# Optimization experiments

Measured on AMD Instinct MI355X. Metric: run time of the kernel, lower is better.

Reference implementation:

```python
import jax, jax.numpy as jnp
import numpy as np

B, S, WD, H, STEP = 32, 512, 512, 512, 2
NG = 8  # gate order: f1, f2, f3, f4, f5, i, o, u


def setup_inputs() -> dict:
    key = jax.random.key(0)
    ks = jax.random.split(key, 12)
    std = 0.1
    word_inputs = jax.random.normal(ks[0], (B, S, WD), jnp.float32)
    position_table = jax.random.randint(ks[1], (B, S), 0, S + 1)  # 0 -> pad row
    mask = jnp.ones((B, S), jnp.int32)
    # nograd uniform(-0.05, 0.05) initial states created inside torch forward
    init_h = jax.random.uniform(ks[2], (B, S, H), jnp.float32, -0.05, 0.05)
    init_c = jax.random.uniform(ks[3], (B, S, H), jnp.float32, -0.05, 0.05)
    Wx = std * jax.random.normal(ks[4], (NG, H, H), jnp.float32)
    Wh = std * jax.random.normal(ks[5], (NG, 2 * H, H), jnp.float32)
    Wi = std * jax.random.normal(ks[6], (NG, WD, H), jnp.float32)
    Wd = std * jax.random.normal(ks[7], (NG, H, H), jnp.float32)
    Ws = std * jax.random.normal(ks[8], (NG, H, H), jnp.float32)
    b = std * jax.random.normal(ks[9], (NG, H), jnp.float32)
    gW = std * jax.random.normal(ks[10], (6, H, H), jnp.float32)  # Wxd,Whd,Wxo,Who,Wxf,Whf
    gb = std * jax.random.normal(ks[11], (3, H), jnp.float32)     # bd,bo,bf
    return dict(word_inputs=word_inputs, init_h=init_h, init_c=init_c,
                Wx=Wx, Wh=Wh, Wi=Wi, Wd=Wd, Ws=Ws, b=b, gW=gW, gb=gb,
                position_table=position_table, mask=mask, num_layers=4)


def _shift_sum_before(x, steps):
    # sum_{s=1..steps} of x right-shifted by s with zero padding at front
    out = jnp.zeros_like(x)
    for s in range(1, steps + 1):
        pad = jnp.zeros(x[:, :s].shape, x.dtype)
        out = out + jnp.concatenate([pad, x[:, :-s]], axis=1)
    return out


def _shift_sum_after(x, steps):
    out = jnp.zeros_like(x)
    for s in range(1, steps + 1):
        pad = jnp.zeros(x[:, :s].shape, x.dtype)
        out = out + jnp.concatenate([x[:, s:], pad], axis=1)
    return out


def _position_switch(x, pos):
    # prepend a zero pad row at position 0, then gather along seq dim
    x_add = jnp.concatenate([jnp.zeros_like(x[:, :1]), x], axis=1)  # [B,S+1,H]
    return jnp.take_along_axis(x_add, pos[:, :, None], axis=1)


def reference(word_inputs, init_h, init_c, Wx, Wh, Wi, Wd, Ws, b, gW, gb,
              position_table, mask, num_layers):
    maskf = mask.astype(jnp.float32)
    seq_mask = maskf[:, :, None]                         # [B,S,1]
    mask_score = (maskf * 1e25 - 1e25)[:, :, None]       # 0 where valid, -1e25 where pad
    emb = (word_inputs * seq_mask).reshape(-1, WD)       # embedding_hidden_state_pre
    h = init_h * seq_mask
    c = init_c * seq_mask
    dummy_h = jnp.mean(h, axis=1)
    dummy_c = jnp.mean(c, axis=1)
    gWxd, gWhd, gWxo, gWho, gWxf, gWhf = gW[0], gW[1], gW[2], gW[3], gW[4], gW[5]
    gbd, gbo, gbf = gb[0], gb[1], gb[2]
    for _ in range(num_layers):
        sw_h = _position_switch(h, position_table)
        sw_c = _position_switch(c, position_table)
        combined = jnp.mean(h, axis=1)                   # [B,H]
        rh = h.reshape(-1, H)                            # [B*S,H]
        td_h = jnp.broadcast_to(dummy_h[:, None], h.shape).reshape(-1, H)
        # dummy (sentence-state) node update
        gd = jax.nn.sigmoid(dummy_h @ gWxd + combined @ gWhd + gbd)
        go = jax.nn.sigmoid(dummy_h @ gWxo + combined @ gWho + gbo)
        gf = jax.nn.sigmoid(td_h @ gWxf + rh @ gWhf + gbf).reshape(h.shape) + mask_score
        scores = jax.nn.softmax(jnp.concatenate([gf, gd[:, None]], axis=1), axis=1)  # [B,S+1,H]
        dummy_c_new = jnp.sum(scores[:, :S] * c, axis=1) + scores[:, S] * dummy_c
        dummy_h_new = go * jnp.tanh(dummy_c_new)
        # neighbor window sums (before/after) for h and c
        hb = _shift_sum_before(h, STEP).reshape(-1, H)
        ha = _shift_sum_after(h, STEP).reshape(-1, H)
        cb = _shift_sum_before(c, STEP).reshape(-1, H)
        ca = _shift_sum_after(c, STEP).reshape(-1, H)
        cat = jnp.concatenate([hb, ha], axis=1)          # [B*S,2H]
        td_c = jnp.broadcast_to(dummy_c[:, None], c.shape).reshape(-1, H)
        sw_hf = sw_h.reshape(-1, H)
        sw_cf = sw_c.reshape(-1, H)
        # all 8 gate pre-activations in stacked einsums: [8,B*S,H]
        z = (jnp.einsum('nh,ghk->gnk', rh, Wx)
             + jnp.einsum('nd,gdk->gnk', cat, Wh)
             + jnp.einsum('nw,gwk->gnk', emb, Wi)
             + jnp.einsum('nh,ghk->gnk', td_h, Wd)
             + jnp.einsum('nh,ghk->gnk', sw_hf, Ws)
             + b[:, None, :])
        gates6 = jax.nn.softmax(jax.nn.sigmoid(z[:6]), axis=0)  # normalize f1..f5,i
        f1, f2, f3, f4, f5, i_t = gates6[0], gates6[1], gates6[2], gates6[3], gates6[4], gates6[5]
        o_t = jax.nn.sigmoid(z[6])
        u_t = jnp.tanh(z[7])
        cf = c.reshape(-1, H)
        c_new = f1 * cb + f2 * ca + f3 * cf + f4 * td_c + f5 * sw_cf + i_t * u_t
        h_new = o_t * jnp.tanh(c_new)
        h = h_new.reshape(B, S, H) * seq_mask
        c = c_new.reshape(B, S, H) * seq_mask
        dummy_h, dummy_c = dummy_h_new, dummy_c_new
    return h
```

## Files before the change

kernel.cpp:

```cpp
#include <hip/hip_runtime.h>
#include <cstddef>

#define Bn 32
#define Sn 512
#define Hn 512
#define Rn (Bn*Sn)
#define NLAYER 4
constexpr size_t NHe = (size_t)Rn * Hn;

typedef __attribute__((ext_vector_type(8))) _Float16 f16x8;
typedef __attribute__((ext_vector_type(4))) float f32x4;

__device__ __forceinline__ float sigf(float x) { return 1.f / (1.f + __expf(-x)); }
__device__ __forceinline__ void gl_lds16(const void* g, void* l) {
  __builtin_amdgcn_global_load_lds((const __attribute__((address_space(1))) void*)g,
                                   (__attribute__((address_space(3))) void*)l, 16, 0, 0);
}
#define VMCNT(n) asm volatile("s_waitcnt vmcnt(" #n ")" ::: "memory")

__global__ void k_init(const float* __restrict__ ih, const float* __restrict__ ic,
                       const int* __restrict__ mask,
                       float* __restrict__ h, float* __restrict__ c) {
  size_t i = (size_t)blockIdx.x * blockDim.x + threadIdx.x;
  size_t n = i >> 7;
  float m = (float)mask[n];
  float4 b = ((const float4*)ih)[i];
  float4 d = ((const float4*)ic)[i];
  b.x *= m; b.y *= m; b.z *= m; b.w *= m;
  d.x *= m; d.y *= m; d.z *= m; d.w *= m;
  ((float4*)h)[i] = b; ((float4*)c)[i] = d;
}

__global__ void k_mean2(const float* __restrict__ x, const float* __restrict__ y,
                        float* __restrict__ ox, float* __restrict__ oy) {
  int idx = blockIdx.x * blockDim.x + threadIdx.x;
  int b = idx >> 9, k = idx & 511;
  const float* px = x + (size_t)b * Sn * Hn + k;
  const float* py = y + (size_t)b * Sn * Hn + k;
  float sx = 0.f, sy = 0.f;
#pragma unroll 8
  for (int t = 0; t < Sn; ++t) { sx += px[(size_t)t * Hn]; sy += py[(size_t)t * Hn]; }
  ox[idx] = sx * (1.f / Sn); oy[idx] = sy * (1.f / Sn);
}

__global__ void k_mean1a(const float* __restrict__ x, float* __restrict__ part) {
  int b = blockIdx.x, sc = blockIdx.y;
  int k4 = threadIdx.x & 127;
  int so = threadIdx.x >> 7;
  const float4* px = (const float4*)x + ((size_t)(b * Sn + sc * 64 + so)) * 128 + k4;
  float4 s = make_float4(0.f, 0.f, 0.f, 0.f);
#pragma unroll 4
  for (int t = 0; t < 32; ++t) {
    float4 v = px[(size_t)t * 256];
    s.x += v.x; s.y += v.y; s.z += v.z; s.w += v.w;
  }
  ((float4*)part)[((size_t)(sc * 2 + so) * Bn + b) * 128 + k4] = s;
}
__global__ void k_mean1b(const float* __restrict__ part, float* __restrict__ comb) {
  int idx = blockIdx.x * blockDim.x + threadIdx.x;
  int b = idx >> 7, k4 = idx & 127;
  float4 s = make_float4(0.f, 0.f, 0.f, 0.f);
#pragma unroll
  for (int p = 0; p < 16; ++p) {
    float4 v = ((const float4*)part)[((size_t)p * Bn + b) * 128 + k4];
    s.x += v.x; s.y += v.y; s.z += v.z; s.w += v.w;
  }
  s.x *= (1.f / Sn); s.y *= (1.f / Sn); s.z *= (1.f / Sn); s.w *= (1.f / Sn);
  ((float4*)comb)[idx] = s;
}

__global__ void k_gates_small(const float* __restrict__ dh, const float* __restrict__ comb,
                              const float* __restrict__ gW, const float* __restrict__ gb,
                              float* __restrict__ gd, float* __restrict__ go,
                              float* __restrict__ gfA) {
  int idx = blockIdx.x * blockDim.x + threadIdx.x;
  int b = idx >> 9, k = idx & 511;
  const float* gW0 = gW;
  const float* gW1 = gW + 1 * Hn * Hn;
  const float* gW2 = gW + 2 * Hn * Hn;
  const float* gW3 = gW + 3 * Hn * Hn;
  const float* gW4 = gW + 4 * Hn * Hn;
  const float* dhb = dh + b * Hn;
  const float* cbp = comb + b * Hn;
  float s0 = 0.f, s1 = 0.f, s2 = 0.f, s3 = 0.f, s4 = 0.f;
#pragma unroll 4
  for (int j = 0; j < Hn; ++j) {
    float a = dhb[j], c2 = cbp[j];
    s0 += a * gW0[j * Hn + k];
    s1 += c2 * gW1[j * Hn + k];
    s2 += a * gW2[j * Hn + k];
    s3 += c2 * gW3[j * Hn + k];
    s4 += a * gW4[j * Hn + k];
  }
  gd[idx] = sigf(s0 + s1 + gb[k]);
  go[idx] = sigf(s2 + s3 + gb[Hn + k]);
  gfA[idx] = s4 + gb[2 * Hn + k];
}

__global__ void k_dWd(const float* __restrict__ dh, const float* __restrict__ Wd,
                      float* __restrict__ dWd) {
  int idx = blockIdx.x * blockDim.x + threadIdx.x;
  int k = idx & 511; int bg = idx >> 9; int b = bg & 31; int g = bg >> 5;
  const float* w = Wd + (size_t)g * Hn * Hn;
  const float* dhb = dh + b * Hn;
  float s = 0.f;
#pragma unroll 4
  for (int j = 0; j < Hn; ++j) s += dhb[j] * w[j * Hn + k];
  dWd[idx] = s;
}

__global__ void k_dummy1(const float* __restrict__ G, const float* __restrict__ gfA,
                         const float* __restrict__ c, const int* __restrict__ mask,
                         float* __restrict__ np_, float* __restrict__ dp_) {
  int b = blockIdx.x, sc = blockIdx.y;
  int k = threadIdx.x;
  float gfa = gfA[(b << 9) | k];
  const float* Gp = G + ((size_t)(b * Sn + sc * 64)) * Hn + k;
  const float* cp = c + ((size_t)(b * Sn + sc * 64)) * Hn + k;
  const int* mp = mask + b * Sn + sc * 64;
  float num = 0.f, den = 0.f;
#pragma unroll 4
  for (int s = 0; s < 64; ++s) {
    float e = __expf(sigf(Gp[(size_t)s * Hn] + gfa));
    e = mp[s] ? e : 0.f;
    num += e * cp[(size_t)s * Hn];
    den += e;
  }
  np_[((size_t)sc * Bn + b) * Hn + k] = num;
  dp_[((size_t)sc * Bn + b) * Hn + k] = den;
}
__global__ void k_dummy2(const float* __restrict__ np_, const float* __restrict__ dp_,
                         const float* __restrict__ gd, const float* __restrict__ go,
                         const float* __restrict__ dc,
                         float* __restrict__ dh2, float* __restrict__ dc2) {
  int idx = blockIdx.x * blockDim.x + threadIdx.x;
  int b = idx >> 9, k = idx & 511;
  float ed = __expf(gd[idx]);
  float num = ed * dc[idx], den = ed;
#pragma unroll
  for (int sc = 0; sc < 8; ++sc) {
    num += np_[((size_t)sc * Bn + b) * Hn + k];
    den += dp_[((size_t)sc * Bn + b) * Hn + k];
  }
  float d = num / den;
  dc2[idx] = d;
  dh2[idx] = go[idx] * tanhf(d);
}

__global__ void k_convw(const float* __restrict__ Wx, const float* __restrict__ Wh,
                        const float* __restrict__ Wsm, const float* __restrict__ Wi,
                        _Float16* __restrict__ Bhat) {
  int kcT = blockIdx.x, nT = blockIdx.y, tg = blockIdx.z;
  int t = tg >> 3, g = tg & 7;
  const float* base;
  if (t == 0)      base = Wx  + (size_t)g * 262144;
  else if (t == 1) base = Wh  + (size_t)g * 524288;
  else if (t == 2) base = Wh  + (size_t)g * 524288 + 262144;
  else if (t == 3) base = Wsm + (size_t)g * 262144;
  else             base = Wi  + (size_t)g * 262144;
  size_t sbase = ((size_t)(t * 16 + nT) * 16 + kcT) * 8192 + (size_t)g * 1024;
  int lane = threadIdx.x;
  for (int cch = lane; cch < 128; cch += 64) {
    int ni = cch >> 6, quad = (cch >> 4) & 3, l15 = cch & 15;
    int n = nT * 32 + ni * 16 + l15;
    int k0 = kcT * 32 + quad * 8;
    f16x8 w8;
#pragma unroll
    for (int j = 0; j < 8; ++j) w8[j] = (_Float16)base[(size_t)(k0 + j) * Hn + n];
    *(f16x8*)&Bhat[sbase + (size_t)cch * 8] = w8;
  }
}

__global__ void k_convG(const float* __restrict__ gW, _Float16* __restrict__ Ghat) {
  int kcT = blockIdx.x, nT4 = blockIdx.y;
  int tid = threadIdx.x;
  const float* w = gW + (size_t)5 * Hn * Hn;
  size_t sb = ((size_t)(nT4 * 16 + kcT)) * 4096;
#pragma unroll
  for (int half = 0; half < 2; ++half) {
    int st = half * 256 + tid;
    int nj = st >> 6, quad = (st >> 4) & 3, l15 = st & 15;
    int n = nT4 * 128 + nj * 16 + l15;
    int k0 = kcT * 32 + quad * 8;
    f16x8 w8;
#pragma unroll
    for (int j = 0; j < 8; ++j) w8[j] = (_Float16)w[(size_t)(k0 + j) * Hn + n];
    *(f16x8*)&Ghat[sb + (size_t)st * 8] = w8;
  }
}

__global__ void k_prepA(const float* __restrict__ h, const int* __restrict__ pos,
                        _Float16* __restrict__ Ahat) {
  const int mb = blockIdx.x, kcT = blockIdx.y, t = blockIdx.z;
  const int tid = threadIdx.x;
  size_t sb = ((size_t)(t * 128 + mb) * 16 + kcT) * 4096;
#pragma unroll
  for (int half = 0; half < 2; ++half) {
    int st = half * 256 + tid;
    int rg = st >> 6, quad = (st >> 4) & 3, l15 = st & 15;
    int r = mb * 128 + rg * 16 + l15;
    int srow = r & (Sn - 1);
    int k0 = kcT * 32 + quad * 8;
    const float* base = h + (size_t)r * Hn + k0;
    float v[8];
    if (t == 0) {
#pragma unroll
      for (int j = 0; j < 8; ++j) v[j] = base[j];
    } else if (t == 1) {
#pragma unroll
      for (int j = 0; j < 8; ++j) v[j] = 0.f;
      if (srow >= 1) { const float* p = base - Hn;
#pragma unroll
        for (int j = 0; j < 8; ++j) v[j] += p[j]; }
      if (srow >= 2) { const float* p = base - 2 * Hn;
#pragma unroll
        for (int j = 0; j < 8; ++j) v[j] += p[j]; }
    } else if (t == 2) {
#pragma unroll
      for (int j = 0; j < 8; ++j) v[j] = 0.f;
      if (srow <= Sn - 2) { const float* p = base + Hn;
#pragma unroll
        for (int j = 0; j < 8; ++j) v[j] += p[j]; }
      if (srow <= Sn - 3) { const float* p = base + 2 * Hn;
#pragma unroll
        for (int j = 0; j < 8; ++j) v[j] += p[j]; }
    } else {
      int pp = pos[r];
      if (pp) {
        const float* p = h + ((size_t)((r >> 9) * Sn + pp - 1)) * Hn + k0;
#pragma unroll
        for (int j = 0; j < 8; ++j) v[j] = p[j];
      } else {
#pragma unroll
        for (int j = 0; j < 8; ++j) v[j] = 0.f;
      }
    }
    f16x8 o8;
#pragma unroll
    for (int j = 0; j < 8; ++j) o8[j] = (_Float16)v[j];
    *(f16x8*)&Ahat[sb + (size_t)st * 8] = o8;
  }
}

__global__ void k_prepW(const float* __restrict__ w, const int* __restrict__ mask,
                        _Float16* __restrict__ Ahat) {
  const int mb = blockIdx.x, kcT = blockIdx.y;
  const int tid = threadIdx.x;
  size_t sb = ((size_t)(4 * 128 + mb) * 16 + kcT) * 4096;
#pragma unroll
  for (int half = 0; half < 2; ++half) {
    int st = half * 256 + tid;
    int rg = st >> 6, quad = (st >> 4) & 3, l15 = st & 15;
    int r = mb * 128 + rg * 16 + l15;
    int k0 = kcT * 32 + quad * 8;
    float mf = (float)mask[r];
    const float* base = w + (size_t)r * Hn + k0;
    f16x8 o8;
#pragma unroll
    for (int j = 0; j < 8; ++j) o8[j] = (_Float16)(base[j] * mf);
    *(f16x8*)&Ahat[sb + (size_t)st * 8] = o8;
  }
}

__global__ __launch_bounds__(256, 3) void k_gemm1(const _Float16* __restrict__ Ahat,
                                                  const _Float16* __restrict__ Ghat,
                                                  float* __restrict__ G) {
  __shared__ _Float16 As[2][4096];
  __shared__ _Float16 Bs[2][4096];
  const int tid = threadIdx.x;
  const int mb = blockIdx.x, nT4 = blockIdx.y;
  const int lane = tid & 63, wid = tid >> 6;
  const int quad = lane >> 4, l15 = lane & 15;
  const int afo0 = (((wid * 2 + 0) * 4 + quad) * 16 + l15) * 8;
  const int afo1 = (((wid * 2 + 1) * 4 + quad) * 16 + l15) * 8;

  f32x4 acc[2][8];
#pragma unroll
  for (int mi = 0; mi < 2; ++mi)
#pragma unroll
    for (int nj = 0; nj < 8; ++nj) acc[mi][nj] = (f32x4){0.f, 0.f, 0.f, 0.f};

  auto stage = [&](int buf, int kcT) {
    const int4* sa = (const int4*)Ahat + ((size_t)(mb * 16 + kcT) << 9);
    const int4* sbp = (const int4*)Ghat + ((size_t)(nT4 * 16 + kcT) << 9);
#pragma unroll
    for (int q = 0; q < 2; ++q) {
      gl_lds16(sa + q * 256 + tid, &As[buf][(q * 256 + tid) * 8]);
      gl_lds16(sbp + q * 256 + tid, &Bs[buf][(q * 256 + tid) * 8]);
    }
  };

  stage(0, 0);
  __syncthreads();
#pragma unroll 1
  for (int kcT = 0; kcT < 16; ++kcT) {
    const int cur = kcT & 1;
    if (kcT < 15) stage(cur ^ 1, kcT + 1);
    f16x8 a0 = *(const f16x8*)&As[cur][afo0];
    f16x8 a1 = *(const f16x8*)&As[cur][afo1];
#pragma unroll
    for (int nj = 0; nj < 8; ++nj) {
      f16x8 bh = *(const f16x8*)&Bs[cur][((nj * 4 + quad) * 16 + l15) * 8];
      acc[0][nj] = __builtin_amdgcn_mfma_f32_16x16x32_f16(a0, bh, acc[0][nj], 0, 0, 0);
      acc[1][nj] = __builtin_amdgcn_mfma_f32_16x16x32_f16(a1, bh, acc[1][nj], 0, 0, 0);
    }
    __syncthreads();
  }
#pragma unroll
  for (int mi = 0; mi < 2; ++mi)
#pragma unroll
    for (int r = 0; r < 4; ++r) {
      int row = mb * 128 + wid * 32 + mi * 16 + quad * 4 + r;
      float* gp = G + (size_t)row * Hn + nT4 * 128 + l15;
#pragma unroll
      for (int nj = 0; nj < 8; ++nj) gp[nj * 16] = acc[mi][nj][r];
    }
}

__global__ __launch_bounds__(512, 2) void k_mega(
    const float* __restrict__ c,
    const _Float16* __restrict__ Ahat, const _Float16* __restrict__ Bhat,
    const int* __restrict__ pos, const int* __restrict__ mask,
    const float* __restrict__ dc, const float* __restrict__ dWd,
    const float* __restrict__ bias,
    float* __restrict__ hout, float* __restrict__ cout) {
  __shared__ _Float16 As[2][16384];
  __shared__ _Float16 Bs[2][16384];

  const int tid = threadIdx.x;
  const int id = blockIdx.x;
  const int xcd = id & 7;
  const int loc = id >> 3;
  const int mt = xcd * 8 + (loc >> 4);
  const int nT = loc & 15;
  const int m0 = mt * 256;
  const int n0 = nT * 32;
  const int bb = m0 >> 9;

  const int lane = tid & 63, wid = tid >> 6;
  const int quad = lane >> 4, l15 = lane & 15;
  const int row_grp = wid >> 1;
  const int col_half = wid & 1;
  const int mb2 = row_grp >> 1;
  const int rg0 = (row_grp & 1) * 4;

  const int afoA0 = (mb2 * 4096) + ((rg0 * 4 + quad) * 16 + l15) * 8;
  const int afoA1 = (2 * 4096 + mb2 * 4096) + ((rg0 * 4 + quad) * 16 + l15) * 8;
  const int bfo = col_half * 512 + quad * 128 + l15 * 8;

  f32x4 acc[8][4];
#pragma unroll
  for (int g = 0; g < 8; ++g)
#pragma unroll
    for (int mi = 0; mi < 4; ++mi) acc[g][mi] = (f32x4){0.f, 0.f, 0.f, 0.f};

  auto stageA = [&](int buf, int kt2) {
    const int t = kt2 >> 3, kc2 = (kt2 & 7) * 2;
#pragma unroll
    for (int kk = 0; kk < 2; ++kk)
#pragma unroll
      for (int m2 = 0; m2 < 2; ++m2) {
        const int4* src = (const int4*)Ahat +
            ((size_t)((t * 128 + mt * 2 + m2) * 16 + kc2 + kk)) * 512;
        gl_lds16(src + tid, &As[buf][(kk * 2 + m2) * 4096 + tid * 8]);
      }
#pragma unroll
    for (int kk = 0; kk < 2; ++kk) {
      const int4* srcb = (const int4*)Bhat +
          ((size_t)((t * 16 + nT) * 16 + kc2 + kk)) * 1024;
      gl_lds16(srcb + tid, &Bs[buf][kk * 8192 + tid * 8]);
    }
  };
  auto stageB = [&](int buf, int kt2) {
    const int t = kt2 >> 3, kc2 = (kt2 & 7) * 2;
#pragma unroll
    for (int kk = 0; kk < 2; ++kk) {
      const int4* srcb = (const int4*)Bhat +
          ((size_t)((t * 16 + nT) * 16 + kc2 + kk)) * 1024 + 512;
      gl_lds16(srcb + tid, &Bs[buf][kk * 8192 + 4096 + tid * 8]);
    }
  };

  stageA(0, 0);
  stageB(0, 0);

#pragma unroll 1
  for (int kt = 0; kt < 40; ++kt) {
    const int cur = kt & 1;
    const int nbuf = cur ^ 1;
    VMCNT(2);
    __builtin_amdgcn_s_barrier();
    f16x8 a[4][2], b[4];
#pragma unroll
    for (int mi = 0; mi < 4; ++mi) {
      a[mi][0] = *(const f16x8*)&As[cur][afoA0 + mi * 512];
      a[mi][1] = *(const f16x8*)&As[cur][afoA1 + mi * 512];
    }
#pragma unroll
    for (int g = 0; g < 4; ++g) b[g] = *(const f16x8*)&Bs[cur][g * 1024 + bfo];
    if (kt < 39) stageA(nbuf, kt + 1);
    asm volatile("s_waitcnt lgkmcnt(0)" ::: "memory");
    __builtin_amdgcn_sched_barrier(0);
    __builtin_amdgcn_s_setprio(1);
#pragma unroll
    for (int g = 0; g < 4; ++g) {
#pragma unroll
      for (int mi = 0; mi < 4; ++mi)
        acc[g][mi] = __builtin_amdgcn_mfma_f32_16x16x32_f16(a[mi][0], b[g], acc[g][mi], 0, 0, 0);
    }
    f16x8 b1[4];
#pragma unroll
    for (int g = 0; g < 4; ++g) b1[g] = *(const f16x8*)&Bs[cur][8192 + g * 1024 + bfo];
    asm volatile("s_waitcnt lgkmcnt(0)" ::: "memory");
    __builtin_amdgcn_sched_barrier(0);
#pragma unroll
    for (int g = 0; g < 4; ++g) {
#pragma unroll
      for (int mi = 0; mi < 4; ++mi)
        acc[g][mi] = __builtin_amdgcn_mfma_f32_16x16x32_f16(a[mi][1], b1[g], acc[g][mi], 0, 0, 0);
    }
    __builtin_amdgcn_s_setprio(0);
    if (kt < 39) { VMCNT(6); }
    else         { VMCNT(0); }
    __builtin_amdgcn_s_barrier();
    f16x8 c0[4], c1[4];
#pragma unroll
    for (int g = 0; g < 4; ++g) {
      c0[g] = *(const f16x8*)&Bs[cur][4096 + g * 1024 + bfo];
      c1[g] = *(const f16x8*)&Bs[cur][8192 + 4096 + g * 1024 + bfo];
    }
    if (kt < 39) stageB(nbuf, kt + 1);
    asm volatile("s_waitcnt lgkmcnt(0)" ::: "memory");
    __builtin_amdgcn_sched_barrier(0);
    __builtin_amdgcn_s_setprio(1);
#pragma unroll
    for (int g = 0; g < 4; ++g) {
#pragma unroll
      for (int mi = 0; mi < 4; ++mi)
        acc[4 + g][mi] = __builtin_amdgcn_mfma_f32_16x16x32_f16(a[mi][0], c0[g], acc[4 + g][mi], 0, 0, 0);
    }
#pragma unroll
    for (int g = 0; g < 4; ++g) {
#pragma unroll
      for (int mi = 0; mi < 4; ++mi)
        acc[4 + g][mi] = __builtin_amdgcn_mfma_f32_16x16x32_f16(a[mi][1], c1[g], acc[4 + g][mi], 0, 0, 0);
    }
    __builtin_amdgcn_s_setprio(0);
    __builtin_amdgcn_s_barrier();
  }

  const int col = n0 + col_half * 16 + l15;
  const float tdcv = dc[bb * Hn + col];
  float biasr[8], dwdr[8];
#pragma unroll
  for (int g = 0; g < 8; ++g) {
    biasr[g] = bias[g * Hn + col];
    dwdr[g] = dWd[((size_t)g * Bn + bb) * Hn + col];
  }

#pragma unroll
  for (int mi = 0; mi < 4; ++mi) {
#pragma unroll
    for (int r = 0; r < 4; ++r) {
      const int row = m0 + row_grp * 64 + mi * 16 + quad * 4 + r;
      const int srow = row & (Sn - 1);
      const float mf = (float)mask[row];
      const int pp = pos[row];
      const size_t rb = (size_t)row * Hn;
      float cf = c[rb + col];
      float cb = 0.f, ca = 0.f;
      if (srow >= 1) cb = c[rb - Hn + col];
      if (srow >= 2) cb += c[rb - 2 * Hn + col];
      if (srow <= Sn - 2) ca = c[rb + Hn + col];
      if (srow <= Sn - 3) ca += c[rb + 2 * Hn + col];
      float sw = pp ? c[((size_t)(bb * Sn + pp - 1)) * Hn + col] : 0.f;
      float z[8];
#pragma unroll
      for (int g = 0; g < 8; ++g)
        z[g] = acc[g][mi][r] + biasr[g] + dwdr[g];
      float e0 = __expf(sigf(z[0]));
      float e1 = __expf(sigf(z[1]));
      float e2 = __expf(sigf(z[2]));
      float e3 = __expf(sigf(z[3]));
      float e4 = __expf(sigf(z[4]));
      float e5 = __expf(sigf(z[5]));
      float inv = 1.f / (e0 + e1 + e2 + e3 + e4 + e5);
      float o = sigf(z[6]);
      float u = tanhf(z[7]);
      float cn = inv * (e0 * cb + e1 * ca + e2 * cf + e3 * tdcv + e4 * sw + e5 * u);
      cout[rb + col] = cn * mf;
      hout[rb + col] = o * tanhf(cn) * mf;
    }
  }
}

extern "C" void kernel_launch(void* const* d_in, const int* in_sizes, int n_in,
                              void* d_out, int out_size, void* d_ws, size_t ws_size,
                              hipStream_t stream) {
  (void)in_sizes; (void)n_in; (void)out_size; (void)ws_size;
  const float* word   = (const float*)d_in[0];
  const float* init_h = (const float*)d_in[1];
  const float* init_c = (const float*)d_in[2];
  const float* Wx     = (const float*)d_in[3];
  const float* Wh     = (const float*)d_in[4];
  const float* Wi     = (const float*)d_in[5];
  const float* Wdm    = (const float*)d_in[6];
  const float* Wsm    = (const float*)d_in[7];
  const float* bias   = (const float*)d_in[8];
  const float* gW     = (const float*)d_in[9];
  const float* gb     = (const float*)d_in[10];
  const int*   pos    = (const int*)d_in[11];
  const int*   mask   = (const int*)d_in[12];

  float* ws = (float*)d_ws;
  size_t off = 0;
  auto alloc = [&](size_t nel) { float* p = ws + off; off += nel; return p; };
  float* cA   = alloc(NHe);
  float* cB   = alloc(NHe);
  float* hS   = alloc(NHe);
  float* G    = hS;
  _Float16* Ahat = (_Float16*)alloc(5 * NHe / 2);
  _Float16* Bhat = (_Float16*)alloc(5 * 8 * 512 * 512 / 2);
  _Float16* Ghat = (_Float16*)alloc(512 * 512 / 2);
  float* part = alloc(16 * Bn * Hn);
  float* np_  = alloc(8 * Bn * Hn);
  float* dp_  = alloc(8 * Bn * Hn);
  float* dh   = alloc(Bn * Hn);
  float* dc   = alloc(Bn * Hn);
  float* dh2  = alloc(Bn * Hn);
  float* dc2  = alloc(Bn * Hn);
  float* comb = alloc(Bn * Hn);
  float* gd   = alloc(Bn * Hn);
  float* go   = alloc(Bn * Hn);
  float* gfA  = alloc(Bn * Hn);
  float* dWd  = alloc(8 * Bn * Hn);

  dim3 blk(256);
  int g4 = (int)(NHe / 4 / 256);
  int gbh = (Bn * Hn) / 256;

  k_convw<<<dim3(16, 16, 40), dim3(64), 0, stream>>>(Wx, Wh, Wsm, Wi, Bhat);
  k_convG<<<dim3(16, 4), blk, 0, stream>>>(gW, Ghat);
  k_prepW<<<dim3(128, 16), blk, 0, stream>>>(word, mask, Ahat);
  k_init<<<g4, blk, 0, stream>>>(init_h, init_c, mask, hS, cA);
  k_mean2<<<gbh, blk, 0, stream>>>(hS, cA, dh, dc);

  float* ccur = cA; float* cnxt = cB;
  for (int l = 0; l < NLAYER; ++l) {
    k_prepA<<<dim3(128, 16, 4), blk, 0, stream>>>(hS, pos, Ahat);
    k_mean1a<<<dim3(Bn, 8), blk, 0, stream>>>(hS, part);
    k_mean1b<<<16, blk, 0, stream>>>(part, comb);
    k_gates_small<<<gbh, blk, 0, stream>>>(dh, comb, gW, gb, gd, go, gfA);
    k_dWd<<<(8 * Bn * Hn) / 256, blk, 0, stream>>>(dh, Wdm, dWd);
    k_gemm1<<<dim3(128, 4), blk, 0, stream>>>(Ahat, Ghat, G);
    k_dummy1<<<dim3(Bn, 8), dim3(512), 0, stream>>>(G, gfA, ccur, mask, np_, dp_);
    k_dummy2<<<gbh, blk, 0, stream>>>(np_, dp_, gd, go, dc, dh2, dc2);

    float* hout = (l == NLAYER - 1) ? (float*)d_out : hS;
    k_mega<<<dim3(1024), dim3(512), 0, stream>>>(
        ccur, Ahat, Bhat, pos, mask, dc, dWd, bias, hout, cnxt);

    float* t1;
    t1 = ccur; ccur = cnxt; cnxt = t1;
    t1 = dh; dh = dh2; dh2 = t1;
    t1 = dc; dc = dc2; dc2 = t1;
  }
}
```

Baseline: 2.276 ms.

## Batch small gate GEMMs on MFMA, fuse dummy reduction into gemm1, merge prepA

The scalar fp32 small-matrix kernels (gates_small, dWd) are replaced by one fp16 MFMA GEMM over 13 stacked weight matrices (5 gate weights plus 8 Wd). This GEMM takes fp16 dh and comb vectors written in MFMA fragment layout, and a tiny elementwise gates kernel follows it. The dummy-node softmax partial sums move into the gemm1 epilogue, so the G matrix is never written to or re-read from global memory. The four prepA variants merge into a single kernel that reads h once and writes all four A tiles. The cost is fp16 precision for the dh/comb and gate projections, and lower occupancy for gemm1 (launch bounds 3 to 2).

After: 1.884 ms. -17.2%, faster.

```diff
diff --git a/kernel.cpp b/kernel.cpp
--- a/kernel.cpp
+++ b/kernel.cpp
@@ -17,6 +17,11 @@
                                    (__attribute__((address_space(3))) void*)l, 16, 0, 0);
 }
 #define VMCNT(n) asm volatile("s_waitcnt vmcnt(" #n ")" ::: "memory")
+
+__device__ __forceinline__ int a32slot(int b, int k) {
+  int kcT = k >> 5, quad = (k >> 3) & 3, j = k & 7, rg = b >> 4, l15 = b & 15;
+  return ((((kcT * 2 + rg) * 4 + quad) * 16 + l15) * 8) + j;
+}
 
 __global__ void k_init(const float* __restrict__ ih, const float* __restrict__ ic,
                        const int* __restrict__ mask,
@@ -32,7 +37,7 @@
 }
 
 __global__ void k_mean2(const float* __restrict__ x, const float* __restrict__ y,
-                        float* __restrict__ ox, float* __restrict__ oy) {
+                        _Float16* __restrict__ dh16, float* __restrict__ oy) {
   int idx = blockIdx.x * blockDim.x + threadIdx.x;
   int b = idx >> 9, k = idx & 511;
   const float* px = x + (size_t)b * Sn * Hn + k;
@@ -40,7 +45,8 @@
   float sx = 0.f, sy = 0.f;
 #pragma unroll 8
   for (int t = 0; t < Sn; ++t) { sx += px[(size_t)t * Hn]; sy += py[(size_t)t * Hn]; }
-  ox[idx] = sx * (1.f / Sn); oy[idx] = sy * (1.f / Sn);
+  oy[idx] = sy * (1.f / Sn);
+  dh16[a32slot(b, k)] = (_Float16)(sx * (1.f / Sn));
 }
 
 __global__ void k_mean1a(const float* __restrict__ x, float* __restrict__ part) {
@@ -56,7 +62,7 @@
   }
   ((float4*)part)[((size_t)(sc * 2 + so) * Bn + b) * 128 + k4] = s;
 }
-__global__ void k_mean1b(const float* __restrict__ part, float* __restrict__ comb) {
+__global__ void k_mean1b(const float* __restrict__ part, _Float16* __restrict__ comb16) {
   int idx = blockIdx.x * blockDim.x + threadIdx.x;
   int b = idx >> 7, k4 = idx & 127;
   float4 s = make_float4(0.f, 0.f, 0.f, 0.f);
@@ -65,86 +71,98 @@
     float4 v = ((const float4*)part)[((size_t)p * Bn + b) * 128 + k4];
     s.x += v.x; s.y += v.y; s.z += v.z; s.w += v.w;
   }
-  s.x *= (1.f / Sn); s.y *= (1.f / Sn); s.z *= (1.f / Sn); s.w *= (1.f / Sn);
-  ((float4*)comb)[idx] = s;
-}
-
-__global__ void k_gates_small(const float* __restrict__ dh, const float* __restrict__ comb,
-                              const float* __restrict__ gW, const float* __restrict__ gb,
-                              float* __restrict__ gd, float* __restrict__ go,
-                              float* __restrict__ gfA) {
+  float vv[4] = {s.x, s.y, s.z, s.w};
+#pragma unroll
+  for (int jj = 0; jj < 4; ++jj)
+    comb16[a32slot(b, k4 * 4 + jj)] = (_Float16)(vv[jj] * (1.f / Sn));
+}
+
+__global__ void k_convS(const float* __restrict__ gW, const float* __restrict__ Wd,
+                        _Float16* __restrict__ Shat) {
+  int kcT = blockIdx.x, nT4 = blockIdx.y, mat = blockIdx.z;
+  int tid = threadIdx.x;
+  const float* w = (mat < 5) ? (gW + (size_t)mat * 262144)
+                             : (Wd + (size_t)(mat - 5) * 262144);
+  size_t sb = ((size_t)((mat * 4 + nT4) * 16 + kcT)) * 4096;
+#pragma unroll
+  for (int half = 0; half < 2; ++half) {
+    int st = half * 256 + tid;
+    int nj = st >> 6, quad = (st >> 4) & 3, l15 = st & 15;
+    int n = nT4 * 128 + nj * 16 + l15;
+    int k0 = kcT * 32 + quad * 8;
+    f16x8 w8;
+#pragma unroll
+    for (int j = 0; j < 8; ++j) w8[j] = (_Float16)w[(size_t)(k0 + j) * Hn + n];
+    *(f16x8*)&Shat[sb + (size_t)st * 8] = w8;
+  }
+}
+
+__global__ __launch_bounds__(256) void k_small(const _Float16* __restrict__ dh16,
+                                               const _Float16* __restrict__ comb16,
+                                               const _Float16* __restrict__ Shat,
+                                               float* __restrict__ S) {
+  const int mat = blockIdx.x, nT4 = blockIdx.y;
+  const int tid = threadIdx.x;
+  const int lane = tid & 63, wid = tid >> 6;
+  const int quad = lane >> 4, l15 = lane & 15;
+  const _Float16* A16 = (mat == 1 || mat == 3) ? comb16 : dh16;
+  const _Float16* Sb = Shat + ((size_t)((mat * 4 + nT4) * 16)) * 4096;
+
+  f32x4 acc[2][2];
+#pragma unroll
+  for (int rg = 0; rg < 2; ++rg)
+#pragma unroll
+    for (int nj = 0; nj < 2; ++nj) acc[rg][nj] = (f32x4){0.f, 0.f, 0.f, 0.f};
+
+#pragma unroll 4
+  for (int kcT = 0; kcT < 16; ++kcT) {
+    f16x8 a0 = *(const f16x8*)&A16[(((kcT * 2 + 0) * 4 + quad) * 16 + l15) * 8];
+    f16x8 a1 = *(const f16x8*)&A16[(((kcT * 2 + 1) * 4 + quad) * 16 + l15) * 8];
+    f16x8 b0 = *(const f16x8*)&Sb[(size_t)kcT * 4096 + (((wid * 2 + 0) * 4 + quad) * 16 + l15) * 8];
+    f16x8 b1 = *(const f16x8*)&Sb[(size_t)kcT * 4096 + (((wid * 2 + 1) * 4 + quad) * 16 + l15) * 8];
+    acc[0][0] = __builtin_amdgcn_mfma_f32_16x16x32_f16(a0, b0, acc[0][0], 0, 0, 0);
+    acc[0][1] = __builtin_amdgcn_mfma_f32_16x16x32_f16(a0, b1, acc[0][1], 0, 0, 0);
+    acc[1][0] = __builtin_amdgcn_mfma_f32_16x16x32_f16(a1, b0, acc[1][0], 0, 0, 0);
+    acc[1][1] = __builtin_amdgcn_mfma_f32_16x16x32_f16(a1, b1, acc[1][1], 0, 0, 0);
+  }
+#pragma unroll
+  for (int rg = 0; rg < 2; ++rg)
+#pragma unroll
+    for (int nj = 0; nj < 2; ++nj)
+#pragma unroll
+      for (int r = 0; r < 4; ++r) {
+        int brow = rg * 16 + quad * 4 + r;
+        int col = nT4 * 128 + (wid * 2 + nj) * 16 + l15;
+        S[(size_t)mat * 16384 + brow * 512 + col] = acc[rg][nj][r];
+      }
+}
+
+__global__ void k_gates2(const float* __restrict__ S, const float* __restrict__ gb,
+                         float* __restrict__ gd, float* __restrict__ go,
+                         float* __restrict__ gfA) {
   int idx = blockIdx.x * blockDim.x + threadIdx.x;
-  int b = idx >> 9, k = idx & 511;
-  const float* gW0 = gW;
-  const float* gW1 = gW + 1 * Hn * Hn;
-  const float* gW2 = gW + 2 * Hn * Hn;
-  const float* gW3 = gW + 3 * Hn * Hn;
-  const float* gW4 = gW + 4 * Hn * Hn;
-  const float* dhb = dh + b * Hn;
-  const float* cbp = comb + b * Hn;
-  float s0 = 0.f, s1 = 0.f, s2 = 0.f, s3 = 0.f, s4 = 0.f;
-#pragma unroll 4
-  for (int j = 0; j < Hn; ++j) {
-    float a = dhb[j], c2 = cbp[j];
-    s0 += a * gW0[j * Hn + k];
-    s1 += c2 * gW1[j * Hn + k];
-    s2 += a * gW2[j * Hn + k];
-    s3 += c2 * gW3[j * Hn + k];
-    s4 += a * gW4[j * Hn + k];
-  }
-  gd[idx] = sigf(s0 + s1 + gb[k]);
-  go[idx] = sigf(s2 + s3 + gb[Hn + k]);
-  gfA[idx] = s4 + gb[2 * Hn + k];
-}
-
-__global__ void k_dWd(const float* __restrict__ dh, const float* __restrict__ Wd,
-                      float* __restrict__ dWd) {
-  int idx = blockIdx.x * blockDim.x + threadIdx.x;
-  int k = idx & 511; int bg = idx >> 9; int b = bg & 31; int g = bg >> 5;
-  const float* w = Wd + (size_t)g * Hn * Hn;
-  const float* dhb = dh + b * Hn;
-  float s = 0.f;
-#pragma unroll 4
-  for (int j = 0; j < Hn; ++j) s += dhb[j] * w[j * Hn + k];
-  dWd[idx] = s;
-}
-
-__global__ void k_dummy1(const float* __restrict__ G, const float* __restrict__ gfA,
-                         const float* __restrict__ c, const int* __restrict__ mask,
-                         float* __restrict__ np_, float* __restrict__ dp_) {
-  int b = blockIdx.x, sc = blockIdx.y;
-  int k = threadIdx.x;
-  float gfa = gfA[(b << 9) | k];
-  const float* Gp = G + ((size_t)(b * Sn + sc * 64)) * Hn + k;
-  const float* cp = c + ((size_t)(b * Sn + sc * 64)) * Hn + k;
-  const int* mp = mask + b * Sn + sc * 64;
-  float num = 0.f, den = 0.f;
-#pragma unroll 4
-  for (int s = 0; s < 64; ++s) {
-    float e = __expf(sigf(Gp[(size_t)s * Hn] + gfa));
-    e = mp[s] ? e : 0.f;
-    num += e * cp[(size_t)s * Hn];
-    den += e;
-  }
-  np_[((size_t)sc * Bn + b) * Hn + k] = num;
-  dp_[((size_t)sc * Bn + b) * Hn + k] = den;
-}
-__global__ void k_dummy2(const float* __restrict__ np_, const float* __restrict__ dp_,
+  int k = idx & 511;
+  gd[idx] = sigf(S[idx] + S[16384 + idx] + gb[k]);
+  go[idx] = sigf(S[2 * 16384 + idx] + S[3 * 16384 + idx] + gb[512 + k]);
+  gfA[idx] = S[4 * 16384 + idx] + gb[1024 + k];
+}
+
+__global__ void k_dummy2(const float* __restrict__ pnum, const float* __restrict__ pden,
                          const float* __restrict__ gd, const float* __restrict__ go,
                          const float* __restrict__ dc,
-                         float* __restrict__ dh2, float* __restrict__ dc2) {
+                         _Float16* __restrict__ dh16o, float* __restrict__ dc2) {
   int idx = blockIdx.x * blockDim.x + threadIdx.x;
   int b = idx >> 9, k = idx & 511;
   float ed = __expf(gd[idx]);
   float num = ed * dc[idx], den = ed;
 #pragma unroll
-  for (int sc = 0; sc < 8; ++sc) {
-    num += np_[((size_t)sc * Bn + b) * Hn + k];
-    den += dp_[((size_t)sc * Bn + b) * Hn + k];
+  for (int q = 0; q < 4; ++q) {
+    num += pnum[(size_t)(b * 4 + q) * 512 + k];
+    den += pden[(size_t)(b * 4 + q) * 512 + k];
   }
   float d = num / den;
   dc2[idx] = d;
-  dh2[idx] = go[idx] * tanhf(d);
+  dh16o[a32slot(b, k)] = (_Float16)(go[idx] * tanhf(d));
 }
 
 __global__ void k_convw(const float* __restrict__ Wx, const float* __restrict__ Wh,
@@ -189,11 +207,10 @@
   }
 }
 
-__global__ void k_prepA(const float* __restrict__ h, const int* __restrict__ pos,
-                        _Float16* __restrict__ Ahat) {
-  const int mb = blockIdx.x, kcT = blockIdx.y, t = blockIdx.z;
+__global__ void k_prepAll(const float* __restrict__ h, const int* __restrict__ pos,
+                          _Float16* __restrict__ Ahat) {
+  const int mb = blockIdx.x, kcT = blockIdx.y;
   const int tid = threadIdx.x;
-  size_t sb = ((size_t)(t * 128 + mb) * 16 + kcT) * 4096;
 #pragma unroll
   for (int half = 0; half < 2; ++half) {
     int st = half * 256 + tid;
@@ -202,43 +219,38 @@
     int srow = r & (Sn - 1);
     int k0 = kcT * 32 + quad * 8;
     const float* base = h + (size_t)r * Hn + k0;
-    float v[8];
-    if (t == 0) {
-#pragma unroll
-      for (int j = 0; j < 8; ++j) v[j] = base[j];
-    } else if (t == 1) {
-#pragma unroll
-      for (int j = 0; j < 8; ++j) v[j] = 0.f;
-      if (srow >= 1) { const float* p = base - Hn;
-#pragma unroll
-        for (int j = 0; j < 8; ++j) v[j] += p[j]; }
-      if (srow >= 2) { const float* p = base - 2 * Hn;
-#pragma unroll
-        for (int j = 0; j < 8; ++j) v[j] += p[j]; }
-    } else if (t == 2) {
-#pragma unroll
-      for (int j = 0; j < 8; ++j) v[j] = 0.f;
-      if (srow <= Sn - 2) { const float* p = base + Hn;
-#pragma unroll
-        for (int j = 0; j < 8; ++j) v[j] += p[j]; }
-      if (srow <= Sn - 3) { const float* p = base + 2 * Hn;
-#pragma unroll
-        for (int j = 0; j < 8; ++j) v[j] += p[j]; }
-    } else {
-      int pp = pos[r];
-      if (pp) {
-        const float* p = h + ((size_t)((r >> 9) * Sn + pp - 1)) * Hn + k0;
-#pragma unroll
-        for (int j = 0; j < 8; ++j) v[j] = p[j];
-      } else {
-#pragma unroll
-        for (int j = 0; j < 8; ++j) v[j] = 0.f;
-      }
-    }
-    f16x8 o8;
-#pragma unroll
-    for (int j = 0; j < 8; ++j) o8[j] = (_Float16)v[j];
-    *(f16x8*)&Ahat[sb + (size_t)st * 8] = o8;
+    float v0[8], v1[8], v2[8], v3[8];
+#pragma unroll
+    for (int j = 0; j < 8; ++j) { v0[j] = base[j]; v1[j] = 0.f; v2[j] = 0.f; v3[j] = 0.f; }
+    if (srow >= 1) { const float* p = base - Hn;
+#pragma unroll
+      for (int j = 0; j < 8; ++j) v1[j] += p[j]; }
+    if (srow >= 2) { const float* p = base - 2 * Hn;
+#pragma unroll
+      for (int j = 0; j < 8; ++j) v1[j] += p[j]; }
+    if (srow <= Sn - 2) { const float* p = base + Hn;
+#pragma unroll
+      for (int j = 0; j < 8; ++j) v2[j] += p[j]; }
+    if (srow <= Sn - 3) { const float* p = base + 2 * Hn;
+#pragma unroll
+      for (int j = 0; j < 8; ++j) v2[j] += p[j]; }
+    int pp = pos[r];
+    if (pp) {
+      const float* p = h + ((size_t)((r >> 9) * Sn + pp - 1)) * Hn + k0;
+#pragma unroll
+      for (int j = 0; j < 8; ++j) v3[j] = p[j];
+    }
+    size_t stoff = (size_t)st * 8;
+    f16x8 o0, o1, o2, o3;
+#pragma unroll
+    for (int j = 0; j < 8; ++j) {
+      o0[j] = (_Float16)v0[j]; o1[j] = (_Float16)v1[j];
+      o2[j] = (_Float16)v2[j]; o3[j] = (_Float16)v3[j];
+    }
+    *(f16x8*)&Ahat[((size_t)(0 * 128 + mb) * 16 + kcT) * 4096 + stoff] = o0;
+    *(f16x8*)&Ahat[((size_t)(1 * 128 + mb) * 16 + kcT) * 4096 + stoff] = o1;
+    *(f16x8*)&Ahat[((size_t)(2 * 128 + mb) * 16 + kcT) * 4096 + stoff] = o2;
+    *(f16x8*)&Ahat[((size_t)(3 * 128 + mb) * 16 + kcT) * 4096 + stoff] = o3;
   }
 }
 
@@ -262,11 +274,16 @@
   }
 }
 
-__global__ __launch_bounds__(256, 3) void k_gemm1(const _Float16* __restrict__ Ahat,
-                                                  const _Float16* __restrict__ Ghat,
-                                                  float* __restrict__ G) {
+__global__ __launch_bounds__(256, 2) void k_gemm1d(const _Float16* __restrict__ Ahat,
+                                                   const _Float16* __restrict__ Ghat,
+                                                   const float* __restrict__ gfA,
+                                                   const float* __restrict__ cbuf,
+                                                   const int* __restrict__ mask,
+                                                   float* __restrict__ pnum,
+                                                   float* __restrict__ pden) {
   __shared__ _Float16 As[2][4096];
   __shared__ _Float16 Bs[2][4096];
+  __shared__ float red[4][2][128];
   const int tid = threadIdx.x;
   const int mb = blockIdx.x, nT4 = blockIdx.y;
   const int lane = tid & 63, wid = tid >> 6;
@@ -306,15 +323,50 @@
     }
     __syncthreads();
   }
-#pragma unroll
-  for (int mi = 0; mi < 2; ++mi)
+
+  const int bb = mb >> 2;
+  float gfa[8], nsum[8], dsum[8];
+#pragma unroll
+  for (int nj = 0; nj < 8; ++nj) {
+    gfa[nj] = gfA[bb * 512 + nT4 * 128 + nj * 16 + l15];
+    nsum[nj] = 0.f; dsum[nj] = 0.f;
+  }
+#pragma unroll
+  for (int mi = 0; mi < 2; ++mi) {
 #pragma unroll
     for (int r = 0; r < 4; ++r) {
       int row = mb * 128 + wid * 32 + mi * 16 + quad * 4 + r;
-      float* gp = G + (size_t)row * Hn + nT4 * 128 + l15;
-#pragma unroll
-      for (int nj = 0; nj < 8; ++nj) gp[nj * 16] = acc[mi][nj][r];
-    }
+      float mf = (float)mask[row];
+      const float* crow = cbuf + (size_t)row * 512 + nT4 * 128 + l15;
+#pragma unroll
+      for (int nj = 0; nj < 8; ++nj) {
+        float e = __expf(sigf(acc[mi][nj][r] + gfa[nj])) * mf;
+        nsum[nj] += e * crow[nj * 16];
+        dsum[nj] += e;
+      }
+    }
+  }
+#pragma unroll
+  for (int nj = 0; nj < 8; ++nj) {
+    nsum[nj] += __shfl_xor(nsum[nj], 16);
+    nsum[nj] += __shfl_xor(nsum[nj], 32);
+    dsum[nj] += __shfl_xor(dsum[nj], 16);
+    dsum[nj] += __shfl_xor(dsum[nj], 32);
+  }
+  if (quad == 0) {
+#pragma unroll
+    for (int nj = 0; nj < 8; ++nj) {
+      red[wid][0][nj * 16 + l15] = nsum[nj];
+      red[wid][1][nj * 16 + l15] = dsum[nj];
+    }
+  }
+  __syncthreads();
+  {
+    int cc = tid & 127, which = tid >> 7;
+    float v = red[0][which][cc] + red[1][which][cc] + red[2][which][cc] + red[3][which][cc];
+    float* dst = which ? pden : pnum;
+    dst[(size_t)mb * 512 + nT4 * 128 + cc] = v;
+  }
 }
 
 __global__ __launch_bounds__(512, 2) void k_mega(
@@ -518,22 +570,22 @@
   float* cA   = alloc(NHe);
   float* cB   = alloc(NHe);
   float* hS   = alloc(NHe);
-  float* G    = hS;
   _Float16* Ahat = (_Float16*)alloc(5 * NHe / 2);
   _Float16* Bhat = (_Float16*)alloc(5 * 8 * 512 * 512 / 2);
   _Float16* Ghat = (_Float16*)alloc(512 * 512 / 2);
+  _Float16* Shat = (_Float16*)alloc(13 * 512 * 512 / 2);
+  float* S    = alloc(13 * 16384);
   float* part = alloc(16 * Bn * Hn);
-  float* np_  = alloc(8 * Bn * Hn);
-  float* dp_  = alloc(8 * Bn * Hn);
-  float* dh   = alloc(Bn * Hn);
+  float* pnum = alloc(128 * 512);
+  float* pden = alloc(128 * 512);
+  _Float16* dh16A = (_Float16*)alloc(8192);
+  _Float16* dh16B = (_Float16*)alloc(8192);
+  _Float16* comb16 = (_Float16*)alloc(8192);
   float* dc   = alloc(Bn * Hn);
-  float* dh2  = alloc(Bn * Hn);
   float* dc2  = alloc(Bn * Hn);
-  float* comb = alloc(Bn * Hn);
   float* gd   = alloc(Bn * Hn);
   float* go   = alloc(Bn * Hn);
   float* gfA  = alloc(Bn * Hn);
-  float* dWd  = alloc(8 * Bn * Hn);
 
   dim3 blk(256);
   int g4 = (int)(NHe / 4 / 256);
@@ -541,28 +593,29 @@
 
   k_convw<<<dim3(16, 16, 40), dim3(64), 0, stream>>>(Wx, Wh, Wsm, Wi, Bhat);
   k_convG<<<dim3(16, 4), blk, 0, stream>>>(gW, Ghat);
+  k_convS<<<dim3(16, 4, 13), blk, 0, stream>>>(gW, Wdm, Shat);
   k_prepW<<<dim3(128, 16), blk, 0, stream>>>(word, mask, Ahat);
   k_init<<<g4, blk, 0, stream>>>(init_h, init_c, mask, hS, cA);
-  k_mean2<<<gbh, blk, 0, stream>>>(hS, cA, dh, dc);
+  k_mean2<<<gbh, blk, 0, stream>>>(hS, cA, dh16A, dc);
 
   float* ccur = cA; float* cnxt = cB;
+  _Float16* dhc = dh16A; _Float16* dhn = dh16B;
   for (int l = 0; l < NLAYER; ++l) {
-    k_prepA<<<dim3(128, 16, 4), blk, 0, stream>>>(hS, pos, Ahat);
+    k_prepAll<<<dim3(128, 16), blk, 0, stream>>>(hS, pos, Ahat);
     k_mean1a<<<dim3(Bn, 8), blk, 0, stream>>>(hS, part);
-    k_mean1b<<<16, blk, 0, stream>>>(part, comb);
-    k_gates_small<<<gbh, blk, 0, stream>>>(dh, comb, gW, gb, gd, go, gfA);
-    k_dWd<<<(8 * Bn * Hn) / 256, blk, 0, stream>>>(dh, Wdm, dWd);
-    k_gemm1<<<dim3(128, 4), blk, 0, stream>>>(Ahat, Ghat, G);
-    k_dummy1<<<dim3(Bn, 8), dim3(512), 0, stream>>>(G, gfA, ccur, mask, np_, dp_);
-    k_dummy2<<<gbh, blk, 0, stream>>>(np_, dp_, gd, go, dc, dh2, dc2);
+    k_mean1b<<<16, blk, 0, stream>>>(part, comb16);
+    k_small<<<dim3(13, 4), blk, 0, stream>>>(dhc, comb16, Shat, S);
+    k_gates2<<<gbh, blk, 0, stream>>>(S, gb, gd, go, gfA);
+    k_gemm1d<<<dim3(128, 4), blk, 0, stream>>>(Ahat, Ghat, gfA, ccur, mask, pnum, pden);
+    k_dummy2<<<gbh, blk, 0, stream>>>(pnum, pden, gd, go, dc, dhn, dc2);
 
     float* hout = (l == NLAYER - 1) ? (float*)d_out : hS;
     k_mega<<<dim3(1024), dim3(512), 0, stream>>>(
-        ccur, Ahat, Bhat, pos, mask, dc, dWd, bias, hout, cnxt);
+        ccur, Ahat, Bhat, pos, mask, dc, S + (size_t)5 * 16384, bias, hout, cnxt);
 
     float* t1;
     t1 = ccur; ccur = cnxt; cnxt = t1;
-    t1 = dh; dh = dh2; dh2 = t1;
     t1 = dc; dc = dc2; dc2 = t1;
-  }
-}
+    _Float16* t2 = dhc; dhc = dhn; dhn = t2;
+  }
+}
```
